# Kernel tuning notes

Measured on AMD Instinct MI355X. Metric: run time of the kernel, lower is better.

The kernel has to match this reference:

```python
import jax, jax.numpy as jnp
import numpy as np

S = 100000   # unique_source_num
T = 20000    # unique_target_num
N = S + T    # total nodes (sources first, then targets)
E = 1000000  # edges
SRC_DIM, EMB_DIM, TGT_DIM = 256, 128, 128


def setup_inputs() -> dict:
    key = jax.random.key(0)
    ks = jax.random.split(key, 6)
    source_feat = jax.random.normal(ks[0], (N, SRC_DIM), dtype=jnp.float32)
    src_idx = jax.random.randint(ks[1], (E,), 0, S)            # edge sources in [0, S)
    dst_idx = jax.random.randint(ks[2], (E,), 0, T)            # edge targets, target-local in [0, T)
    range_list = jax.random.randint(ks[3], (T, 2), 0, S)       # unused by the math (passed through in torch)
    # x_norm divides features; keep it bounded away from 0 like real row norms
    x_norm = jax.random.uniform(ks[4], (N,), dtype=jnp.float32, minval=0.5, maxval=1.5)
    k_e, k_w = jax.random.split(ks[5])
    embed = jax.random.normal(k_e, (SRC_DIM, EMB_DIM), dtype=jnp.float32)          # Param, std=1 init
    weight = jax.random.normal(k_w, (EMB_DIM, TGT_DIM), dtype=jnp.float32) / np.sqrt(EMB_DIM)  # is_after_relu std=1/sqrt(in)
    return {"source_feat": source_feat, "src_idx": src_idx, "dst_idx": dst_idx,
            "range_list": range_list, "x_norm": x_norm, "embed": embed, "weight": weight}


def reference(source_feat, src_idx, dst_idx, range_list, x_norm, embed, weight):
    # x = (source_feat @ embed) / x_norm[:, None]   -> [N, EMB_DIM]
    x = jnp.matmul(source_feat, embed) / x_norm[:, None]
    # message + scatter-mean aggregation onto targets (sources receive no edges,
    # so aggregating directly over the T targets == aggr_out[S:] in the torch code)
    msgs = x[src_idx]                                           # [E, EMB_DIM] gather
    summed = jax.ops.segment_sum(msgs, dst_idx, num_segments=T) # [T, EMB_DIM]
    cnt = jax.ops.segment_sum(jnp.ones((E,), dtype=x.dtype), dst_idx, num_segments=T)
    aggr = summed / jnp.maximum(cnt, 1.0)[:, None]              # mean; zero-degree -> 0
    out = jnp.matmul(aggr, weight)                              # [T, TGT_DIM]
    return out
```

## Files before the change

kernel.cpp:

```cpp
#include <hip/hip_runtime.h>
#include <cstdint>
#include <cstddef>

#define S_NUM 100000
#define T_NUM 20000
#define E_NUM 1000000

#define NB   1250
#define GT   16
#define CAP  1280
#define CH   4096
#define KB2  245
#define KB1  1563

typedef __bf16 bf16x8 __attribute__((ext_vector_type(8)));
typedef float f32x4 __attribute__((ext_vector_type(4)));

__device__ __forceinline__ unsigned short f2bf(float f) {
  unsigned int u = __float_as_uint(f);
  u += 0x7fffu + ((u >> 16) & 1u);
  return (unsigned short)(u >> 16);
}
__device__ __forceinline__ unsigned int f2bf2(float lo, float hi) {
  return (unsigned int)f2bf(lo) | ((unsigned int)f2bf(hi) << 16);
}
__device__ __forceinline__ float bflo(unsigned int v) { return __uint_as_float(v << 16); }
__device__ __forceinline__ float bfhi(unsigned int v) { return __uint_as_float(v & 0xffff0000u); }

__launch_bounds__(256)
__global__ void k0_prep(const float* __restrict__ embed, const float* __restrict__ weight,
                        int* __restrict__ gcursor, unsigned short* __restrict__ embedT,
                        unsigned short* __restrict__ weightT) {
  const int idx = blockIdx.x * 256 + threadIdx.x;
  if (idx < 2048) gcursor[idx] = 0;
  {
    const int col = idx & 127;
    const int k = idx >> 7;
    embedT[(size_t)col * 256 + k] = f2bf(embed[(size_t)k * 128 + col]);
  }
  if (idx < 16384) {
    const int n = idx & 127;
    const int k = idx >> 7;
    weightT[(size_t)n * 128 + k] = f2bf(weight[(size_t)k * 128 + n]);
  }
}

__launch_bounds__(512, 8)
__global__ void k12_fused(const float* __restrict__ sf, const float* __restrict__ xn,
                          const unsigned short* __restrict__ embedT, unsigned short* __restrict__ xb,
                          const int* __restrict__ src_idx, const int* __restrict__ dst_idx,
                          int* __restrict__ gcursor, unsigned int* __restrict__ ebuf) {
  __shared__ __align__(16) unsigned char smem[64 * 296 * 2];
  const int tid = threadIdx.x;

  if (blockIdx.x < KB2) {
    int* bcnt  = (int*)smem;
    int* gbase = (int*)(smem + 5120);
    const int e0 = blockIdx.x * CH;
    const int e1 = (e0 + CH < E_NUM) ? (e0 + CH) : E_NUM;
    for (int i = tid; i < NB; i += 512) bcnt[i] = 0;
    __syncthreads();
    for (int e = e0 + tid; e < e1; e += 512)
      atomicAdd(&bcnt[dst_idx[e] >> 4], 1);
    __syncthreads();
    for (int i = tid; i < NB; i += 512) {
      const int cnt = bcnt[i];
      gbase[i] = (cnt > 0) ? atomicAdd(&gcursor[i], cnt) : 0;
      bcnt[i] = 0;
    }
    __syncthreads();
    for (int e = e0 + tid; e < e1; e += 512) {
      const int d = dst_idx[e];
      const int s = src_idx[e];
      const int b = d >> 4;
      const int r = atomicAdd(&bcnt[b], 1);
      const int pos = gbase[b] + r;
      if (pos < CAP)
        ebuf[(size_t)b * CAP + pos] = ((unsigned int)(d & 15) << 17) | (unsigned int)s;
    }
    return;
  }

  unsigned short (*lA)[296] = (unsigned short (*)[296])smem;
  unsigned short (*lC)[136] = (unsigned short (*)[136])smem;
  const int wave = tid >> 6;
  const int lane = tid & 63;
  const int quad = lane >> 4;
  const int l15 = lane & 15;
  const int row0 = (blockIdx.x - KB2) * 64;
  const int col0 = wave * 16;
  const unsigned short* ebT = embedT + (size_t)(col0 + l15) * 256;

#pragma unroll
  for (int i = 0; i < 4; ++i) {
    const int idx = i * 512 + tid;
    const int row = idx >> 5;
    const int seg = idx & 31;
    const float4* g = (const float4*)(sf + (size_t)(row0 + row) * 256 + seg * 8);
    const float4 v0 = g[0];
    const float4 v1 = g[1];
    uint4 pk;
    pk.x = f2bf2(v0.x, v0.y);
    pk.y = f2bf2(v0.z, v0.w);
    pk.z = f2bf2(v1.x, v1.y);
    pk.w = f2bf2(v1.z, v1.w);
    *(uint4*)&lA[row][seg * 8] = pk;
  }
  bf16x8 fbn = *(const bf16x8*)(ebT + quad * 8);
  __syncthreads();

  f32x4 acc[4];
#pragma unroll
  for (int i = 0; i < 4; ++i) acc[i] = (f32x4){0.f, 0.f, 0.f, 0.f};

#pragma unroll
  for (int kc = 0; kc < 8; ++kc) {
    const bf16x8 fbc = fbn;
    if (kc < 7) fbn = *(const bf16x8*)(ebT + (kc + 1) * 32 + quad * 8);
#pragma unroll
    for (int rt = 0; rt < 4; ++rt) {
      bf16x8 fa = *(const bf16x8*)&lA[rt * 16 + l15][kc * 32 + quad * 8];
      acc[rt] = __builtin_amdgcn_mfma_f32_16x16x32_bf16(fa, fbc, acc[rt], 0, 0, 0);
    }
  }
  __syncthreads();

#pragma unroll
  for (int rt = 0; rt < 4; ++rt) {
#pragma unroll
    for (int reg = 0; reg < 4; ++reg) {
      const int row = rt * 16 + quad * 4 + reg;
      const float inv = __builtin_amdgcn_rcpf(xn[row0 + row]);
      lC[row][col0 + l15] = f2bf(acc[rt][reg] * inv);
    }
  }
  __syncthreads();

#pragma unroll
  for (int p = 0; p < 2; ++p) {
    const int i = p * 512 + tid;
    const int row = i >> 4;
    const int seg = i & 15;
    const int gr = row0 + row;
    if (gr < S_NUM)
      *(uint4*)(xb + (size_t)gr * 128 + seg * 8) = *(const uint4*)&lC[row][seg * 8];
  }
}

__launch_bounds__(512, 8)
__global__ void k3_fused(const int* __restrict__ gcursor, const unsigned int* __restrict__ ebuf,
                         const unsigned short* __restrict__ xb,
                         const unsigned short* __restrict__ weightT,
                         float* __restrict__ out) {
  __shared__ unsigned int sls[CAP];
  __shared__ int hist[GT], scn[GT], cur[GT];
  __shared__ unsigned int Pu[GT][68];
  const int b = blockIdx.x;
  const int tid = threadIdx.x;
  const int wave = tid >> 6, lane = tid & 63;
  const int quad = lane >> 4, l15 = lane & 15;

  int n = gcursor[b];
  if (n > CAP) n = CAP;
  const unsigned int* eb = ebuf + (size_t)b * CAP;

  if (tid < GT) hist[tid] = 0;
  __syncthreads();
  for (int i = tid; i < n; i += 512) atomicAdd(&hist[eb[i] >> 17], 1);
  __syncthreads();
  if (tid == 0) {
    int run = 0;
#pragma unroll
    for (int i = 0; i < GT; ++i) { scn[i] = run; run += hist[i]; }
  }
  __syncthreads();
  if (tid < GT) cur[tid] = scn[tid];
  __syncthreads();
  for (int i = tid; i < n; i += 512) {
    const unsigned int e = eb[i];
    const int r = atomicAdd(&cur[e >> 17], 1);
    sls[r] = e & 0x1FFFFu;
  }
  __syncthreads();

  const int h = lane >> 5;
  const int cq = lane & 31;
#pragma unroll
  for (int rep = 0; rep < 2; ++rep) {
    const int tl = wave * 2 + rep;
    const int beg = scn[tl];
    const int c = hist[tl];
    float t0 = 0.f, t1 = 0.f, t2 = 0.f, t3 = 0.f;
    int e = 0;
    if (c >= 16) {
      int scur[8];
#pragma unroll
      for (int j = 0; j < 8; ++j) scur[j] = (int)sls[beg + 2 * j + h];
      for (; e + 32 <= c; e += 16) {
        uint2 v[8];
#pragma unroll
        for (int j = 0; j < 8; ++j)
          v[j] = *(const uint2*)(xb + (size_t)scur[j] * 128 + 4 * cq);
        int snext[8];
#pragma unroll
        for (int j = 0; j < 8; ++j)
          snext[j] = (int)sls[beg + e + 16 + 2 * j + h];
#pragma unroll
        for (int j = 0; j < 8; ++j) {
          t0 += bflo(v[j].x); t1 += bfhi(v[j].x);
          t2 += bflo(v[j].y); t3 += bfhi(v[j].y);
        }
#pragma unroll
        for (int j = 0; j < 8; ++j) scur[j] = snext[j];
      }
      {
        uint2 v[8];
#pragma unroll
        for (int j = 0; j < 8; ++j)
          v[j] = *(const uint2*)(xb + (size_t)scur[j] * 128 + 4 * cq);
#pragma unroll
        for (int j = 0; j < 8; ++j) {
          t0 += bflo(v[j].x); t1 += bfhi(v[j].x);
          t2 += bflo(v[j].y); t3 += bfhi(v[j].y);
        }
        e += 16;
      }
    }
    for (; e + 2 <= c; e += 2) {
      const int s0 = (int)sls[beg + e + h];
      const uint2 v0 = *(const uint2*)(xb + (size_t)s0 * 128 + 4 * cq);
      t0 += bflo(v0.x); t1 += bfhi(v0.x);
      t2 += bflo(v0.y); t3 += bfhi(v0.y);
    }
    if ((c & 1) && h == 0) {
      const int s0 = (int)sls[beg + c - 1];
      const uint2 v0 = *(const uint2*)(xb + (size_t)s0 * 128 + 4 * cq);
      t0 += bflo(v0.x); t1 += bfhi(v0.x);
      t2 += bflo(v0.y); t3 += bfhi(v0.y);
    }
    t0 += __shfl_xor(t0, 32, 64);
    t1 += __shfl_xor(t1, 32, 64);
    t2 += __shfl_xor(t2, 32, 64);
    t3 += __shfl_xor(t3, 32, 64);
    const float inv = (c > 0) ? __builtin_amdgcn_rcpf((float)c) : 0.f;
    const unsigned int pk = h ? f2bf2(t2 * inv, t3 * inv) : f2bf2(t0 * inv, t1 * inv);
    Pu[tl][2 * cq + h] = pk;
  }
  __syncthreads();

  const int ncol = wave * 16 + l15;
  const unsigned short* wT = weightT + (size_t)ncol * 128;
  bf16x8 wb[4];
#pragma unroll
  for (int kc = 0; kc < 4; ++kc)
    wb[kc] = *(const bf16x8*)(wT + kc * 32 + quad * 8);
  f32x4 o0 = (f32x4){0.f, 0.f, 0.f, 0.f};
#pragma unroll
  for (int kc = 0; kc < 4; ++kc) {
    bf16x8 p0 = *(const bf16x8*)((const unsigned short*)&Pu[l15][0] + kc * 32 + quad * 8);
    o0 = __builtin_amdgcn_mfma_f32_16x16x32_bf16(p0, wb[kc], o0, 0, 0, 0);
  }
#pragma unroll
  for (int reg = 0; reg < 4; ++reg)
    out[((size_t)b * GT + quad * 4 + reg) * 128 + ncol] = o0[reg];
}

extern "C" void kernel_launch(void* const* d_in, const int* in_sizes, int n_in,
                              void* d_out, int out_size, void* d_ws, size_t ws_size,
                              hipStream_t stream) {
  const float* sf      = (const float*)d_in[0];
  const int*   src_idx = (const int*)d_in[1];
  const int*   dst_idx = (const int*)d_in[2];
  const float* xn      = (const float*)d_in[4];
  const float* embed   = (const float*)d_in[5];
  const float* weight  = (const float*)d_in[6];
  float* out = (float*)d_out;

  char* w = (char*)d_ws;
  unsigned short* xb      = (unsigned short*)(w);
  int* gcursor            = (int*)(w + 25600000);
  unsigned int* ebuf      = (unsigned int*)(w + 25608192);
  unsigned short* embedT  = (unsigned short*)(w + 32008192);
  unsigned short* weightT = (unsigned short*)(w + 32073728);

  k0_prep<<<128, 256, 0, stream>>>(embed, weight, gcursor, embedT, weightT);
  k12_fused<<<KB2 + KB1, 512, 0, stream>>>(sf, xn, embedT, xb, src_idx, dst_idx, gcursor, ebuf);
  k3_fused<<<NB, 512, 0, stream>>>(gcursor, ebuf, xb, weightT, out);
}
```

Measured before the change: 252.0 us.

## Split k12 GEMM staging into halves and double-buffer k3 gather loads

The embedding GEMM now stages only the first half of K into LDS. The second half is loaded into registers and converted while the first-half MFMAs run, overlapping global-load latency with compute. The gather-sum loop in k3 is restructured into two register buffers (A/B) so that two batches of 16 edge loads are in flight at once. It also drops the occupancy hints in launch_bounds and uses raw barriers. The cost is higher register pressure, which may reduce occupancy.

```diff
diff --git a/kernel.cpp b/kernel.cpp
--- a/kernel.cpp
+++ b/kernel.cpp
@@ -45,7 +45,6 @@
   }
 }
 
-__launch_bounds__(512, 8)
 __global__ void k12_fused(const float* __restrict__ sf, const float* __restrict__ xn,
                           const unsigned short* __restrict__ embedT, unsigned short* __restrict__ xb,
                           const int* __restrict__ src_idx, const int* __restrict__ dst_idx,
@@ -92,11 +91,11 @@
   const unsigned short* ebT = embedT + (size_t)(col0 + l15) * 256;
 
 #pragma unroll
-  for (int i = 0; i < 4; ++i) {
+  for (int i = 0; i < 2; ++i) {
     const int idx = i * 512 + tid;
-    const int row = idx >> 5;
-    const int seg = idx & 31;
-    const float4* g = (const float4*)(sf + (size_t)(row0 + row) * 256 + seg * 8);
+    const int row = idx >> 4;
+    const int sg  = idx & 15;
+    const float4* g = (const float4*)(sf + (size_t)(row0 + row) * 256 + sg * 8);
     const float4 v0 = g[0];
     const float4 v1 = g[1];
     uint4 pk;
@@ -104,17 +103,59 @@
     pk.y = f2bf2(v0.z, v0.w);
     pk.z = f2bf2(v1.x, v1.y);
     pk.w = f2bf2(v1.z, v1.w);
-    *(uint4*)&lA[row][seg * 8] = pk;
+    *(uint4*)&lA[row][sg * 8] = pk;
+  }
+  float4 b00, b01, b10, b11;
+  {
+    const int r0 = tid >> 4, s0 = tid & 15;
+    const float4* g0 = (const float4*)(sf + (size_t)(row0 + r0) * 256 + 128 + s0 * 8);
+    b00 = g0[0]; b01 = g0[1];
+    const int idx1 = 512 + tid;
+    const int r1 = idx1 >> 4, s1 = idx1 & 15;
+    const float4* g1 = (const float4*)(sf + (size_t)(row0 + r1) * 256 + 128 + s1 * 8);
+    b10 = g1[0]; b11 = g1[1];
   }
   bf16x8 fbn = *(const bf16x8*)(ebT + quad * 8);
-  __syncthreads();
+
+  asm volatile("s_waitcnt lgkmcnt(0)" ::: "memory");
+  __builtin_amdgcn_s_barrier();
 
   f32x4 acc[4];
 #pragma unroll
   for (int i = 0; i < 4; ++i) acc[i] = (f32x4){0.f, 0.f, 0.f, 0.f};
 
 #pragma unroll
-  for (int kc = 0; kc < 8; ++kc) {
+  for (int kc = 0; kc < 4; ++kc) {
+    const bf16x8 fbc = fbn;
+    fbn = *(const bf16x8*)(ebT + (kc + 1) * 32 + quad * 8);
+#pragma unroll
+    for (int rt = 0; rt < 4; ++rt) {
+      bf16x8 fa = *(const bf16x8*)&lA[rt * 16 + l15][kc * 32 + quad * 8];
+      acc[rt] = __builtin_amdgcn_mfma_f32_16x16x32_bf16(fa, fbc, acc[rt], 0, 0, 0);
+    }
+  }
+
+  {
+    const int r0 = tid >> 4, s0 = tid & 15;
+    uint4 pk;
+    pk.x = f2bf2(b00.x, b00.y);
+    pk.y = f2bf2(b00.z, b00.w);
+    pk.z = f2bf2(b01.x, b01.y);
+    pk.w = f2bf2(b01.z, b01.w);
+    *(uint4*)&lA[r0][128 + s0 * 8] = pk;
+    const int idx1 = 512 + tid;
+    const int r1 = idx1 >> 4, s1 = idx1 & 15;
+    pk.x = f2bf2(b10.x, b10.y);
+    pk.y = f2bf2(b10.z, b10.w);
+    pk.z = f2bf2(b11.x, b11.y);
+    pk.w = f2bf2(b11.z, b11.w);
+    *(uint4*)&lA[r1][128 + s1 * 8] = pk;
+  }
+  asm volatile("s_waitcnt lgkmcnt(0)" ::: "memory");
+  __builtin_amdgcn_s_barrier();
+
+#pragma unroll
+  for (int kc = 4; kc < 8; ++kc) {
     const bf16x8 fbc = fbn;
     if (kc < 7) fbn = *(const bf16x8*)(ebT + (kc + 1) * 32 + quad * 8);
 #pragma unroll
@@ -147,7 +188,7 @@
   }
 }
 
-__launch_bounds__(512, 8)
+__launch_bounds__(512)
 __global__ void k3_fused(const int* __restrict__ gcursor, const unsigned int* __restrict__ ebuf,
                          const unsigned short* __restrict__ xb,
                          const unsigned short* __restrict__ weightT,
@@ -192,39 +233,85 @@
     const int c = hist[tl];
     float t0 = 0.f, t1 = 0.f, t2 = 0.f, t3 = 0.f;
     int e = 0;
-    if (c >= 16) {
-      int scur[8];
-#pragma unroll
-      for (int j = 0; j < 8; ++j) scur[j] = (int)sls[beg + 2 * j + h];
-      for (; e + 32 <= c; e += 16) {
-        uint2 v[8];
-#pragma unroll
-        for (int j = 0; j < 8; ++j)
-          v[j] = *(const uint2*)(xb + (size_t)scur[j] * 128 + 4 * cq);
-        int snext[8];
-#pragma unroll
-        for (int j = 0; j < 8; ++j)
-          snext[j] = (int)sls[beg + e + 16 + 2 * j + h];
-#pragma unroll
-        for (int j = 0; j < 8; ++j) {
-          t0 += bflo(v[j].x); t1 += bfhi(v[j].x);
-          t2 += bflo(v[j].y); t3 += bfhi(v[j].y);
-        }
-#pragma unroll
-        for (int j = 0; j < 8; ++j) scur[j] = snext[j];
+    const int nb = c >> 4;
+    if (nb >= 2) {
+      int sA[8], sB[8];
+      uint2 vA[8], vB[8];
+#pragma unroll
+      for (int j = 0; j < 8; ++j) sA[j] = (int)sls[beg + 2 * j + h];
+#pragma unroll
+      for (int j = 0; j < 8; ++j) vA[j] = *(const uint2*)(xb + (size_t)sA[j] * 128 + 4 * cq);
+#pragma unroll
+      for (int j = 0; j < 8; ++j) sB[j] = (int)sls[beg + 16 + 2 * j + h];
+#pragma unroll
+      for (int j = 0; j < 8; ++j) vB[j] = *(const uint2*)(xb + (size_t)sB[j] * 128 + 4 * cq);
+      int bi = 0;
+      for (; bi + 3 < nb; bi += 2) {
+#pragma unroll
+        for (int j = 0; j < 8; ++j) {
+          t0 += bflo(vA[j].x); t1 += bfhi(vA[j].x);
+          t2 += bflo(vA[j].y); t3 += bfhi(vA[j].y);
+        }
+#pragma unroll
+        for (int j = 0; j < 8; ++j) sA[j] = (int)sls[beg + (bi + 2) * 16 + 2 * j + h];
+#pragma unroll
+        for (int j = 0; j < 8; ++j) vA[j] = *(const uint2*)(xb + (size_t)sA[j] * 128 + 4 * cq);
+#pragma unroll
+        for (int j = 0; j < 8; ++j) {
+          t0 += bflo(vB[j].x); t1 += bfhi(vB[j].x);
+          t2 += bflo(vB[j].y); t3 += bfhi(vB[j].y);
+        }
+#pragma unroll
+        for (int j = 0; j < 8; ++j) sB[j] = (int)sls[beg + (bi + 3) * 16 + 2 * j + h];
+#pragma unroll
+        for (int j = 0; j < 8; ++j) vB[j] = *(const uint2*)(xb + (size_t)sB[j] * 128 + 4 * cq);
       }
-      {
-        uint2 v[8];
-#pragma unroll
-        for (int j = 0; j < 8; ++j)
-          v[j] = *(const uint2*)(xb + (size_t)scur[j] * 128 + 4 * cq);
-#pragma unroll
-        for (int j = 0; j < 8; ++j) {
-          t0 += bflo(v[j].x); t1 += bfhi(v[j].x);
-          t2 += bflo(v[j].y); t3 += bfhi(v[j].y);
-        }
-        e += 16;
+      if (nb - bi == 3) {
+#pragma unroll
+        for (int j = 0; j < 8; ++j) {
+          t0 += bflo(vA[j].x); t1 += bfhi(vA[j].x);
+          t2 += bflo(vA[j].y); t3 += bfhi(vA[j].y);
+        }
+#pragma unroll
+        for (int j = 0; j < 8; ++j) sA[j] = (int)sls[beg + (bi + 2) * 16 + 2 * j + h];
+#pragma unroll
+        for (int j = 0; j < 8; ++j) vA[j] = *(const uint2*)(xb + (size_t)sA[j] * 128 + 4 * cq);
+#pragma unroll
+        for (int j = 0; j < 8; ++j) {
+          t0 += bflo(vB[j].x); t1 += bfhi(vB[j].x);
+          t2 += bflo(vB[j].y); t3 += bfhi(vB[j].y);
+        }
+#pragma unroll
+        for (int j = 0; j < 8; ++j) {
+          t0 += bflo(vA[j].x); t1 += bfhi(vA[j].x);
+          t2 += bflo(vA[j].y); t3 += bfhi(vA[j].y);
+        }
+      } else {
+#pragma unroll
+        for (int j = 0; j < 8; ++j) {
+          t0 += bflo(vA[j].x); t1 += bfhi(vA[j].x);
+          t2 += bflo(vA[j].y); t3 += bfhi(vA[j].y);
+        }
+#pragma unroll
+        for (int j = 0; j < 8; ++j) {
+          t0 += bflo(vB[j].x); t1 += bfhi(vB[j].x);
+          t2 += bflo(vB[j].y); t3 += bfhi(vB[j].y);
+        }
       }
+      e = nb * 16;
+    } else if (nb == 1) {
+      int s[8];
+#pragma unroll
+      for (int j = 0; j < 8; ++j) s[j] = (int)sls[beg + 2 * j + h];
+      uint2 v[8];
+#pragma unroll
+      for (int j = 0; j < 8; ++j) v[j] = *(const uint2*)(xb + (size_t)s[j] * 128 + 4 * cq);
+#pragma unroll
+      for (int j = 0; j < 8; ++j) {
+        t0 += bflo(v[j].x); t1 += bfhi(v[j].x);
+        t2 += bflo(v[j].y); t3 += bfhi(v[j].y);
+      }
+      e = 16;
     }
     for (; e + 2 <= c; e += 2) {
       const int s0 = (int)sls[beg + e + h];
```

Result: slower. 269.9 us (+7.1%).
